# Kernel optimization log

Measured on AMD Instinct MI355X. Metric: run time of the kernel, lower is better.

The kernel has to match this reference:

```python
import jax, jax.numpy as jnp
import numpy as np

B, H, W, C = 4, 64, 64, 256
CK = C // 8          # 32, f/g projection dim
COUT = 256           # channels_out


def setup_inputs() -> dict:
    key = jax.random.key(0)
    ks = jax.random.split(key, 6)
    s = lambda fan_in: 1.0 / np.sqrt(fan_in)
    return {
        "x": jax.random.normal(ks[0], (B, H, W, C), dtype=jnp.float32),
        "Wf": jax.random.normal(ks[1], (C, CK), dtype=jnp.float32) * s(C),
        "bf": jnp.zeros((CK,), dtype=jnp.float32),
        "Wg": jax.random.normal(ks[2], (C, CK), dtype=jnp.float32) * s(C),
        "bg": jnp.zeros((CK,), dtype=jnp.float32),
        "Wh": jax.random.normal(ks[3], (C, COUT), dtype=jnp.float32) * s(C),
        "bh": jnp.zeros((COUT,), dtype=jnp.float32),
        "Wo": jax.random.normal(ks[4], (COUT, COUT), dtype=jnp.float32) * s(COUT),
        "bo": jnp.zeros((COUT,), dtype=jnp.float32),
        "gamma": jnp.zeros((1,), dtype=jnp.float32),
    }


def reference(x, Wf, bf, Wg, bg, Wh, bh, Wo, bo, gamma):
    b, h, w, c = x.shape
    n = h * w
    xf = x.reshape(b, n, c)                       # [B, N, C]
    # 1x1 convs == per-location dense projections
    f = xf @ Wf + bf                              # [B, N, CK]
    g = xf @ Wg + bg                              # [B, N, CK]
    hh = xf @ Wh + bh                             # [B, N, COUT]
    scores = jnp.einsum("bqk,bnk->bqn", f, g)    # [B, N, N]
    probs = jax.nn.softmax(scores, axis=-1)
    attn = jnp.einsum("bqn,bnd->bqd", probs, hh)  # [B, N, COUT]
    o = attn @ Wo + bo                            # [B, N, COUT]
    y = gamma * o.reshape(b, h, w, -1) + x
    return y
```

## Files before the change

### kernel.cpp

```cpp
#include <hip/hip_runtime.h>
#include <stdint.h>

typedef __attribute__((ext_vector_type(4))) float f32x4;
typedef __attribute__((ext_vector_type(2))) float f32x2;
typedef __attribute__((ext_vector_type(8))) short bf16x8;
typedef __attribute__((ext_vector_type(4))) unsigned short u16x4;

#define NB 4
#define NN 4096
#define CC 256

__device__ __forceinline__ unsigned short f2bf(float f) {
  union { float f; unsigned int u; } v; v.f = f;
  unsigned int u = v.u;
  return (unsigned short)((u + 0x7FFFu + ((u >> 16) & 1u)) >> 16);
}
__device__ __forceinline__ float bf2f(unsigned short h) {
  union { unsigned int u; float f; } v; v.u = ((unsigned int)h) << 16;
  return v.f;
}

__global__ __launch_bounds__(64) void k_wprep(
    const float* __restrict__ Wf, const float* __restrict__ Wg,
    const float* __restrict__ Wh, const float* __restrict__ Wo,
    unsigned short* __restrict__ wT, unsigned short* __restrict__ woT)
{
  const int n = blockIdx.x;
  const int l = threadIdx.x;
  const float* src; int nout, col; unsigned short* dst; int drow;
  if (n < 32)       { src = Wf; nout = 32;  col = n;       dst = wT;  drow = n; }
  else if (n < 64)  { src = Wg; nout = 32;  col = n - 32;  dst = wT;  drow = n; }
  else if (n < 320) { src = Wh; nout = 256; col = n - 64;  dst = wT;  drow = n; }
  else              { src = Wo; nout = 256; col = n - 320; dst = woT; drow = n - 320; }
  u16x4 v;
  #pragma unroll
  for (int j = 0; j < 4; ++j)
    v[j] = f2bf(src[(size_t)(4 * l + j) * nout + col]);
  *(u16x4*)&dst[(size_t)drow * 256 + 4 * l] = v;
}

__global__ __launch_bounds__(256) void k_proj(
    const float* __restrict__ x, const unsigned short* __restrict__ wT,
    const float* __restrict__ bf_, const float* __restrict__ bg_,
    const float* __restrict__ bh_,
    unsigned short* __restrict__ fo, unsigned short* __restrict__ go,
    unsigned short* __restrict__ vT)
{
  __shared__ __align__(16) unsigned short xs[32][264];

  const int t = threadIdx.x, w = t >> 6, l = t & 63;
  const int h = l >> 4, q = l & 15;
  const int bid = blockIdx.x;
  const int rt = (bid & 7) * 64 + (bid >> 3);
  const int r0 = rt * 32;

  #pragma unroll
  for (int p = 0; p < 8; ++p) {
    int idx = t + (p << 8);
    int rr = idx >> 6, c4 = (idx & 63) << 2;
    f32x4 v = *(const f32x4*)&x[(size_t)(r0 + rr) * 256 + c4];
    u16x4 o;
    #pragma unroll
    for (int j = 0; j < 4; ++j) o[j] = f2bf(v[j]);
    *(u16x4*)&xs[rr][c4] = o;
  }
  __syncthreads();

  const f32x4 zero = {0.f, 0.f, 0.f, 0.f};
  f32x4 acc[2][5];
  #pragma unroll
  for (int mf = 0; mf < 2; ++mf)
    #pragma unroll
    for (int nf = 0; nf < 5; ++nf) acc[mf][nf] = zero;

  #pragma unroll
  for (int ks = 0; ks < 8; ++ks) {
    bf16x8 a0 = *(const bf16x8*)&xs[q][ks * 32 + 8 * h];
    bf16x8 a1 = *(const bf16x8*)&xs[16 + q][ks * 32 + 8 * h];
    #pragma unroll
    for (int nf = 0; nf < 5; ++nf) {
      bf16x8 b = *(const bf16x8*)&wT[(size_t)(80 * w + 16 * nf + q) * 256 + ks * 32 + 8 * h];
      acc[0][nf] = __builtin_amdgcn_mfma_f32_16x16x32_bf16(a0, b, acc[0][nf], 0, 0, 0);
      acc[1][nf] = __builtin_amdgcn_mfma_f32_16x16x32_bf16(a1, b, acc[1][nf], 0, 0, 0);
    }
  }

  __syncthreads();

  #pragma unroll
  for (int nf = 0; nf < 5; ++nf) {
    const int colb = 80 * w + 16 * nf;
    const int colq = colb + q;
    #pragma unroll
    for (int mf = 0; mf < 2; ++mf) {
      #pragma unroll
      for (int i = 0; i < 4; ++i) {
        int lr = 16 * mf + 4 * h + i;
        float val = acc[mf][nf][i];
        if (colb < 32) {
          fo[(size_t)(r0 + lr) * 32 + colq] =
              f2bf((val + bf_[colq]) * 1.44269504088896f);
        } else if (colb < 64) {
          go[(size_t)(r0 + lr) * 32 + (colq - 32)] = f2bf(val + bg_[colq - 32]);
        } else {
          xs[lr][colq - 64] = f2bf(val + bh_[colq - 64]);
        }
      }
    }
  }
  __syncthreads();

  const int tile = rt >> 1, sfix = rt & 1;
  unsigned short* dst = vT + (size_t)tile * 16384;
  #pragma unroll
  for (int p = 0; p < 4; ++p) {
    int ci = t + (p << 8);
    int dt = ci >> 6, ll = ci & 63;
    int h2 = (ci >> 4) & 3, q2 = ci & 15;
    bf16x8 v;
    #pragma unroll
    for (int i = 0; i < 8; ++i)
      v[i] = (short)xs[8 * h2 + i][dt * 16 + q2];
    *(bf16x8*)&dst[(size_t)(dt * 128 + sfix * 64 + ll) * 8] = v;
  }
}

#define SM_FIXED_MAX 72.0f

#define ATTN_TILE(KT, VCUR, VNXT, CUR)                                          \
  {                                                                             \
                   \
    f32x4 s0 = __builtin_amdgcn_mfma_f32_16x16x32_bf16(afrag[0], bfj, zero, 0, 0, 0); \
    f32x4 s1 = __builtin_amdgcn_mfma_f32_16x16x32_bf16(afrag[1], bfj, zero, 0, 0, 0); \
    if ((KT) < 63)                                                              \
      bfj = *(const bf16x8*)&gbase[(size_t)(((KT) + 1) * 64 + jst * 16 + q) * 32 + 8 * h]; \
          \
    _Pragma("unroll")                                                           \
    for (int i = 0; i < 4; ++i) {                                               \
      float p0 = exp2f(s0[i] - SM_FIXED_MAX);                                   \
      float p1 = exp2f(s1[i] - SM_FIXED_MAX);                                   \
      lrow[0][i] += p0;                                                         \
      lrow[1][i] += p1;                                                         \
      int slot = (ph2 * 16 + 4 * h + i) * 8 + pi2;                              \
      pbuf[CUR][sec0 * 512 + slot] = (unsigned short)(__float_as_uint(p0) >> 16); \
      pbuf[CUR][sec1 * 512 + slot] = (unsigned short)(__float_as_uint(p1) >> 16); \
    }                                                                           \
    asm volatile("s_waitcnt lgkmcnt(0)" ::: "memory");                          \
    __builtin_amdgcn_s_barrier();                                               \
    __builtin_amdgcn_sched_barrier(0);                                          \
       \
    if ((KT) < 63) {                                                            \
      const unsigned short* vs = vbase + (size_t)((KT) + 1) * 16384;            \
      VNXT[0] = *(const bf16x8*)(vs + (size_t)(dt0 * 128 + l) * 8);             \
      VNXT[1] = *(const bf16x8*)(vs + (size_t)(dt0 * 128 + 64 + l) * 8);        \
      VNXT[2] = *(const bf16x8*)(vs + (size_t)(dt1 * 128 + l) * 8);             \
      VNXT[3] = *(const bf16x8*)(vs + (size_t)(dt1 * 128 + 64 + l) * 8);        \
    }                                                                           \
                             \
    __builtin_amdgcn_s_setprio(1);                                              \
    _Pragma("unroll")                                                           \
    for (int uu = 0; uu < 4; ++uu) {                                            \
      bf16x8 pa0 = *(const bf16x8*)&pbuf[CUR][(uu * 2 + 0) * 512 + l * 8];      \
      bf16x8 pa1 = *(const bf16x8*)&pbuf[CUR][(uu * 2 + 1) * 512 + l * 8];      \
      acc[uu][0] = __builtin_amdgcn_mfma_f32_16x16x32_bf16(pa0, VCUR[0], acc[uu][0], 0, 0, 0); \
      acc[uu][0] = __builtin_amdgcn_mfma_f32_16x16x32_bf16(pa1, VCUR[1], acc[uu][0], 0, 0, 0); \
      acc[uu][1] = __builtin_amdgcn_mfma_f32_16x16x32_bf16(pa0, VCUR[2], acc[uu][1], 0, 0, 0); \
      acc[uu][1] = __builtin_amdgcn_mfma_f32_16x16x32_bf16(pa1, VCUR[3], acc[uu][1], 0, 0, 0); \
    }                                                                           \
    __builtin_amdgcn_s_setprio(0);                                              \
  }

__global__ __launch_bounds__(512, 2) void k_attn(
    const unsigned short* __restrict__ fq,
    const unsigned short* __restrict__ gk,
    const unsigned short* __restrict__ vT,
    float* __restrict__ attn)
{
  __shared__ __align__(16) unsigned short pbuf[2][4096];
  __shared__ float lred[4][4][16];

  const int bid = blockIdx.x;
  const int b  = (bid & 7) >> 1;
  const int qt = (bid >> 3) + ((bid & 1) << 5);
  const int t = threadIdx.x, w = t >> 6, l = t & 63;
  const int h = l >> 4, q = l & 15;
  const int qrow = qt * 64;

  const int uh  = w & 1;
  const int jst = w >> 1;
  const int dt0 = 2 * w, dt1 = 2 * w + 1;

  bf16x8 afrag[2];
  #pragma unroll
  for (int uu = 0; uu < 2; ++uu)
    afrag[uu] = *(const bf16x8*)
        &fq[((size_t)b * NN + qrow + (2 * uh + uu) * 16 + q) * 32 + 8 * h];

  const f32x4 zero = {0.f, 0.f, 0.f, 0.f};
  f32x4 acc[4][2];
  #pragma unroll
  for (int uu = 0; uu < 4; ++uu)
    #pragma unroll
    for (int dl = 0; dl < 2; ++dl) acc[uu][dl] = zero;
  float lrow[2][4];
  #pragma unroll
  for (int uu = 0; uu < 2; ++uu)
    #pragma unroll
    for (int i = 0; i < 4; ++i) lrow[uu][i] = 0.f;

  const unsigned short* gbase = gk + (size_t)b * NN * 32;
  const unsigned short* vbase = vT + (size_t)b * 64 * 16384;

  const int kcol = jst * 16 + q;
  const int ps = kcol >> 5, ph2 = (kcol & 31) >> 3, pi2 = kcol & 7;
  const int sec0 = (2 * uh + 0) * 2 + ps;
  const int sec1 = (2 * uh + 1) * 2 + ps;

  bf16x8 vA[4], vB[4];
  vA[0] = *(const bf16x8*)(vbase + (size_t)(dt0 * 128 + l) * 8);
  vA[1] = *(const bf16x8*)(vbase + (size_t)(dt0 * 128 + 64 + l) * 8);
  vA[2] = *(const bf16x8*)(vbase + (size_t)(dt1 * 128 + l) * 8);
  vA[3] = *(const bf16x8*)(vbase + (size_t)(dt1 * 128 + 64 + l) * 8);
  bf16x8 bfj = *(const bf16x8*)&gbase[(size_t)(jst * 16 + q) * 32 + 8 * h];

  #pragma unroll 1
  for (int kt = 0; kt < 64; kt += 2) {
    ATTN_TILE(kt,     vA, vB, 0);
    ATTN_TILE(kt + 1, vB, vA, 1);
  }

  #pragma unroll
  for (int uu = 0; uu < 2; ++uu)
    #pragma unroll
    for (int i = 0; i < 4; ++i)
      #pragma unroll
      for (int d = 1; d < 16; d <<= 1)
        lrow[uu][i] += __shfl_xor(lrow[uu][i], d);

  if (q == 0) {
    #pragma unroll
    for (int uu = 0; uu < 2; ++uu)
      #pragma unroll
      for (int i = 0; i < 4; ++i)
        lred[jst][2 * uh + uu][4 * h + i] = lrow[uu][i];
  }
  __syncthreads();

  float rl[4][4];
  #pragma unroll
  for (int uu = 0; uu < 4; ++uu)
    #pragma unroll
    for (int i = 0; i < 4; ++i) {
      int row = 4 * h + i;
      rl[uu][i] = 1.0f / (lred[0][uu][row] + lred[1][uu][row] +
                          lred[2][uu][row] + lred[3][uu][row]);
    }

  #pragma unroll
  for (int uu = 0; uu < 4; ++uu)
    #pragma unroll
    for (int dl = 0; dl < 2; ++dl) {
      int dt = 2 * w + dl;
      #pragma unroll
      for (int i = 0; i < 4; ++i)
        attn[((size_t)b * NN + qrow + uu * 16 + 4 * h + i) * 256 + dt * 16 + q] =
            acc[uu][dl][i] * rl[uu][i];
    }
}

__global__ __launch_bounds__(256) void k_out(
    const unsigned short* __restrict__ woT, const float* __restrict__ bo,
    const float* __restrict__ gamma, const float* __restrict__ x,
    float* __restrict__ y)
{
  __shared__ __align__(16) unsigned short as_[32][264];

  const int t = threadIdx.x, w = t >> 6, l = t & 63;
  const int h = l >> 4, q = l & 15;
  const int bid = blockIdx.x;
  const int rt = (bid & 7) * 64 + (bid >> 3);
  const int r0 = rt * 32;

  #pragma unroll
  for (int p = 0; p < 8; ++p) {
    int idx = t + (p << 8);
    int rr = idx >> 6, c4 = (idx & 63) << 2;
    f32x4 v = *(const f32x4*)&y[(size_t)(r0 + rr) * 256 + c4];
    u16x4 o;
    #pragma unroll
    for (int j = 0; j < 4; ++j) o[j] = f2bf(v[j]);
    *(u16x4*)&as_[rr][c4] = o;
  }
  __syncthreads();

  const f32x4 zero = {0.f, 0.f, 0.f, 0.f};
  f32x4 acc[2][4];
  #pragma unroll
  for (int mf = 0; mf < 2; ++mf)
    #pragma unroll
    for (int nf = 0; nf < 4; ++nf) acc[mf][nf] = zero;

  #pragma unroll
  for (int ks = 0; ks < 8; ++ks) {
    bf16x8 a0 = *(const bf16x8*)&as_[q][ks * 32 + 8 * h];
    bf16x8 a1 = *(const bf16x8*)&as_[16 + q][ks * 32 + 8 * h];
    #pragma unroll
    for (int nf = 0; nf < 4; ++nf) {
      bf16x8 b = *(const bf16x8*)&woT[(size_t)(64 * w + 16 * nf + q) * 256 + ks * 32 + 8 * h];
      acc[0][nf] = __builtin_amdgcn_mfma_f32_16x16x32_bf16(a0, b, acc[0][nf], 0, 0, 0);
      acc[1][nf] = __builtin_amdgcn_mfma_f32_16x16x32_bf16(a1, b, acc[1][nf], 0, 0, 0);
    }
  }

  const float gm = gamma[0];
  #pragma unroll
  for (int mf = 0; mf < 2; ++mf)
    #pragma unroll
    for (int nf = 0; nf < 4; ++nf) {
      int col = 64 * w + 16 * nf + q;
      #pragma unroll
      for (int i = 0; i < 4; ++i) {
        size_t off = (size_t)(r0 + 16 * mf + 4 * h + i) * 256 + col;
        y[off] = gm * (acc[mf][nf][i] + bo[col]) + x[off];
      }
    }
}

extern "C" void kernel_launch(void* const* d_in, const int* in_sizes, int n_in,
                              void* d_out, int out_size, void* d_ws, size_t ws_size,
                              hipStream_t stream) {
  const float* x     = (const float*)d_in[0];
  const float* Wf    = (const float*)d_in[1];
  const float* bf_   = (const float*)d_in[2];
  const float* Wg    = (const float*)d_in[3];
  const float* bg_   = (const float*)d_in[4];
  const float* Wh    = (const float*)d_in[5];
  const float* bh_   = (const float*)d_in[6];
  const float* Wo    = (const float*)d_in[7];
  const float* bo    = (const float*)d_in[8];
  const float* gamma = (const float*)d_in[9];

  unsigned short* f   = (unsigned short*)d_ws;
  unsigned short* g   = f   + (size_t)16384 * 32;
  unsigned short* vT  = g   + (size_t)16384 * 32;
  unsigned short* wT  = vT  + (size_t)16384 * 256;
  unsigned short* woT = wT  + (size_t)320 * 256;

  float* attn = (float*)d_out;

  k_wprep<<<576, 64, 0, stream>>>(Wf, Wg, Wh, Wo, wT, woT);
  k_proj<<<512, 256, 0, stream>>>(x, wT, bf_, bg_, bh_, f, g, vT);
  k_attn<<<256, 512, 0, stream>>>(f, g, vT, attn);
  k_out<<<512, 256, 0, stream>>>(woT, bo, gamma, x, attn);
}
```

Measured before the change: 109.1 us.

## Process two key tiles per barrier, stagger tile order, pass bf16 attn to out-proj

The attention loop now handles two 64-key tiles per step, which halves the number of LDS barriers. It prefetches both V tiles and both G fragments for the next step before the softmax work, and starts each block's key sweep at an offset based on its query tile so blocks touch different K/V tiles at the same time. The attention output is written as bf16 to a workspace buffer instead of fp32 into the output tensor, so k_out loads half as many bytes and skips its conversion. In exchange it doubles the LDS P buffer and raises register pressure from eight V fragments per buffer, which may lower occupancy.

```diff
diff --git a/kernel.cpp b/kernel.cpp
--- a/kernel.cpp
+++ b/kernel.cpp
@@ -127,45 +127,64 @@
 
 #define SM_FIXED_MAX 72.0f
 
-#define ATTN_TILE(KT, VCUR, VNXT, CUR)                                          \
+#define ATTN_STEP(ST, VP, VN, GP, GN, CUR)                                      \
   {                                                                             \
-                   \
-    f32x4 s0 = __builtin_amdgcn_mfma_f32_16x16x32_bf16(afrag[0], bfj, zero, 0, 0, 0); \
-    f32x4 s1 = __builtin_amdgcn_mfma_f32_16x16x32_bf16(afrag[1], bfj, zero, 0, 0, 0); \
-    if ((KT) < 63)                                                              \
-      bfj = *(const bf16x8*)&gbase[(size_t)(((KT) + 1) * 64 + jst * 16 + q) * 32 + 8 * h]; \
-          \
+                                                    \
+    f32x4 sA0 = __builtin_amdgcn_mfma_f32_16x16x32_bf16(afrag[0], GP[0], zero, 0, 0, 0); \
+    f32x4 sA1 = __builtin_amdgcn_mfma_f32_16x16x32_bf16(afrag[1], GP[0], zero, 0, 0, 0); \
+    f32x4 sB0 = __builtin_amdgcn_mfma_f32_16x16x32_bf16(afrag[0], GP[1], zero, 0, 0, 0); \
+    f32x4 sB1 = __builtin_amdgcn_mfma_f32_16x16x32_bf16(afrag[1], GP[1], zero, 0, 0, 0); \
+                                   \
+    if ((ST) + 1 < 32) {                                                        \
+      const int kA = (2 * (ST) + 2 + qt) & 63;                                  \
+      const int kB = (2 * (ST) + 3 + qt) & 63;                                  \
+      const unsigned short* vsA = vbase + (size_t)kA * 16384;                   \
+      const unsigned short* vsB = vbase + (size_t)kB * 16384;                   \
+      VN[0] = *(const bf16x8*)(vsA + (size_t)(dt0 * 128 + l) * 8);              \
+      VN[1] = *(const bf16x8*)(vsA + (size_t)(dt0 * 128 + 64 + l) * 8);         \
+      VN[2] = *(const bf16x8*)(vsA + (size_t)(dt1 * 128 + l) * 8);              \
+      VN[3] = *(const bf16x8*)(vsA + (size_t)(dt1 * 128 + 64 + l) * 8);         \
+      VN[4] = *(const bf16x8*)(vsB + (size_t)(dt0 * 128 + l) * 8);              \
+      VN[5] = *(const bf16x8*)(vsB + (size_t)(dt0 * 128 + 64 + l) * 8);         \
+      VN[6] = *(const bf16x8*)(vsB + (size_t)(dt1 * 128 + l) * 8);              \
+      VN[7] = *(const bf16x8*)(vsB + (size_t)(dt1 * 128 + 64 + l) * 8);         \
+      GN[0] = *(const bf16x8*)&gbase[(size_t)(kA * 64 + jst * 16 + q) * 32 + 8 * h]; \
+      GN[1] = *(const bf16x8*)&gbase[(size_t)(kB * 64 + jst * 16 + q) * 32 + 8 * h]; \
+    }                                                                           \
+                     \
     _Pragma("unroll")                                                           \
     for (int i = 0; i < 4; ++i) {                                               \
-      float p0 = exp2f(s0[i] - SM_FIXED_MAX);                                   \
-      float p1 = exp2f(s1[i] - SM_FIXED_MAX);                                   \
-      lrow[0][i] += p0;                                                         \
-      lrow[1][i] += p1;                                                         \
+      float pA0 = exp2f(sA0[i] - SM_FIXED_MAX);                                 \
+      float pA1 = exp2f(sA1[i] - SM_FIXED_MAX);                                 \
+      float pB0 = exp2f(sB0[i] - SM_FIXED_MAX);                                 \
+      float pB1 = exp2f(sB1[i] - SM_FIXED_MAX);                                 \
+      lrow[0][i] += pA0 + pB0;                                                  \
+      lrow[1][i] += pA1 + pB1;                                                  \
       int slot = (ph2 * 16 + 4 * h + i) * 8 + pi2;                              \
-      pbuf[CUR][sec0 * 512 + slot] = (unsigned short)(__float_as_uint(p0) >> 16); \
-      pbuf[CUR][sec1 * 512 + slot] = (unsigned short)(__float_as_uint(p1) >> 16); \
+      pbuf[CUR][sec0 * 512 + slot]        = (unsigned short)(__float_as_uint(pA0) >> 16); \
+      pbuf[CUR][sec1 * 512 + slot]        = (unsigned short)(__float_as_uint(pA1) >> 16); \
+      pbuf[CUR][4096 + sec0 * 512 + slot] = (unsigned short)(__float_as_uint(pB0) >> 16); \
+      pbuf[CUR][4096 + sec1 * 512 + slot] = (unsigned short)(__float_as_uint(pB1) >> 16); \
     }                                                                           \
     asm volatile("s_waitcnt lgkmcnt(0)" ::: "memory");                          \
     __builtin_amdgcn_s_barrier();                                               \
     __builtin_amdgcn_sched_barrier(0);                                          \
-       \
-    if ((KT) < 63) {                                                            \
-      const unsigned short* vs = vbase + (size_t)((KT) + 1) * 16384;            \
-      VNXT[0] = *(const bf16x8*)(vs + (size_t)(dt0 * 128 + l) * 8);             \
-      VNXT[1] = *(const bf16x8*)(vs + (size_t)(dt0 * 128 + 64 + l) * 8);        \
-      VNXT[2] = *(const bf16x8*)(vs + (size_t)(dt1 * 128 + l) * 8);             \
-      VNXT[3] = *(const bf16x8*)(vs + (size_t)(dt1 * 128 + 64 + l) * 8);        \
-    }                                                                           \
-                             \
+             \
     __builtin_amdgcn_s_setprio(1);                                              \
     _Pragma("unroll")                                                           \
     for (int uu = 0; uu < 4; ++uu) {                                            \
-      bf16x8 pa0 = *(const bf16x8*)&pbuf[CUR][(uu * 2 + 0) * 512 + l * 8];      \
-      bf16x8 pa1 = *(const bf16x8*)&pbuf[CUR][(uu * 2 + 1) * 512 + l * 8];      \
-      acc[uu][0] = __builtin_amdgcn_mfma_f32_16x16x32_bf16(pa0, VCUR[0], acc[uu][0], 0, 0, 0); \
-      acc[uu][0] = __builtin_amdgcn_mfma_f32_16x16x32_bf16(pa1, VCUR[1], acc[uu][0], 0, 0, 0); \
-      acc[uu][1] = __builtin_amdgcn_mfma_f32_16x16x32_bf16(pa0, VCUR[2], acc[uu][1], 0, 0, 0); \
-      acc[uu][1] = __builtin_amdgcn_mfma_f32_16x16x32_bf16(pa1, VCUR[3], acc[uu][1], 0, 0, 0); \
+      bf16x8 paA0 = *(const bf16x8*)&pbuf[CUR][(uu * 2 + 0) * 512 + l * 8];     \
+      bf16x8 paA1 = *(const bf16x8*)&pbuf[CUR][(uu * 2 + 1) * 512 + l * 8];     \
+      bf16x8 paB0 = *(const bf16x8*)&pbuf[CUR][4096 + (uu * 2 + 0) * 512 + l * 8]; \
+      bf16x8 paB1 = *(const bf16x8*)&pbuf[CUR][4096 + (uu * 2 + 1) * 512 + l * 8]; \
+      acc[uu][0] = __builtin_amdgcn_mfma_f32_16x16x32_bf16(paA0, VP[0], acc[uu][0], 0, 0, 0); \
+      acc[uu][0] = __builtin_amdgcn_mfma_f32_16x16x32_bf16(paA1, VP[1], acc[uu][0], 0, 0, 0); \
+      acc[uu][0] = __builtin_amdgcn_mfma_f32_16x16x32_bf16(paB0, VP[4], acc[uu][0], 0, 0, 0); \
+      acc[uu][0] = __builtin_amdgcn_mfma_f32_16x16x32_bf16(paB1, VP[5], acc[uu][0], 0, 0, 0); \
+      acc[uu][1] = __builtin_amdgcn_mfma_f32_16x16x32_bf16(paA0, VP[2], acc[uu][1], 0, 0, 0); \
+      acc[uu][1] = __builtin_amdgcn_mfma_f32_16x16x32_bf16(paA1, VP[3], acc[uu][1], 0, 0, 0); \
+      acc[uu][1] = __builtin_amdgcn_mfma_f32_16x16x32_bf16(paB0, VP[6], acc[uu][1], 0, 0, 0); \
+      acc[uu][1] = __builtin_amdgcn_mfma_f32_16x16x32_bf16(paB1, VP[7], acc[uu][1], 0, 0, 0); \
     }                                                                           \
     __builtin_amdgcn_s_setprio(0);                                              \
   }
@@ -174,9 +193,9 @@
     const unsigned short* __restrict__ fq,
     const unsigned short* __restrict__ gk,
     const unsigned short* __restrict__ vT,
-    float* __restrict__ attn)
+    unsigned short* __restrict__ ab)
 {
-  __shared__ __align__(16) unsigned short pbuf[2][4096];
+  __shared__ __align__(16) unsigned short pbuf[2][8192];
   __shared__ float lred[4][4][16];
 
   const int bid = blockIdx.x;
@@ -216,17 +235,27 @@
   const int sec0 = (2 * uh + 0) * 2 + ps;
   const int sec1 = (2 * uh + 1) * 2 + ps;
 
-  bf16x8 vA[4], vB[4];
-  vA[0] = *(const bf16x8*)(vbase + (size_t)(dt0 * 128 + l) * 8);
-  vA[1] = *(const bf16x8*)(vbase + (size_t)(dt0 * 128 + 64 + l) * 8);
-  vA[2] = *(const bf16x8*)(vbase + (size_t)(dt1 * 128 + l) * 8);
-  vA[3] = *(const bf16x8*)(vbase + (size_t)(dt1 * 128 + 64 + l) * 8);
-  bf16x8 bfj = *(const bf16x8*)&gbase[(size_t)(jst * 16 + q) * 32 + 8 * h];
+  const int kp0 = qt & 63, kp1 = (qt + 1) & 63;
+  bf16x8 vX[8], vY[8], gX[2], gY[2];
+  {
+    const unsigned short* vsA = vbase + (size_t)kp0 * 16384;
+    const unsigned short* vsB = vbase + (size_t)kp1 * 16384;
+    vX[0] = *(const bf16x8*)(vsA + (size_t)(dt0 * 128 + l) * 8);
+    vX[1] = *(const bf16x8*)(vsA + (size_t)(dt0 * 128 + 64 + l) * 8);
+    vX[2] = *(const bf16x8*)(vsA + (size_t)(dt1 * 128 + l) * 8);
+    vX[3] = *(const bf16x8*)(vsA + (size_t)(dt1 * 128 + 64 + l) * 8);
+    vX[4] = *(const bf16x8*)(vsB + (size_t)(dt0 * 128 + l) * 8);
+    vX[5] = *(const bf16x8*)(vsB + (size_t)(dt0 * 128 + 64 + l) * 8);
+    vX[6] = *(const bf16x8*)(vsB + (size_t)(dt1 * 128 + l) * 8);
+    vX[7] = *(const bf16x8*)(vsB + (size_t)(dt1 * 128 + 64 + l) * 8);
+    gX[0] = *(const bf16x8*)&gbase[(size_t)(kp0 * 64 + jst * 16 + q) * 32 + 8 * h];
+    gX[1] = *(const bf16x8*)&gbase[(size_t)(kp1 * 64 + jst * 16 + q) * 32 + 8 * h];
+  }
 
   #pragma unroll 1
-  for (int kt = 0; kt < 64; kt += 2) {
-    ATTN_TILE(kt,     vA, vB, 0);
-    ATTN_TILE(kt + 1, vB, vA, 1);
+  for (int st = 0; st < 32; st += 2) {
+    ATTN_STEP(st,     vX, vY, gX, gY, 0);
+    ATTN_STEP(st + 1, vY, vX, gY, gX, 1);
   }
 
   #pragma unroll
@@ -263,15 +292,15 @@
       int dt = 2 * w + dl;
       #pragma unroll
       for (int i = 0; i < 4; ++i)
-        attn[((size_t)b * NN + qrow + uu * 16 + 4 * h + i) * 256 + dt * 16 + q] =
-            acc[uu][dl][i] * rl[uu][i];
+        ab[((size_t)b * NN + qrow + uu * 16 + 4 * h + i) * 256 + dt * 16 + q] =
+            f2bf(acc[uu][dl][i] * rl[uu][i]);
     }
 }
 
 __global__ __launch_bounds__(256) void k_out(
     const unsigned short* __restrict__ woT, const float* __restrict__ bo,
     const float* __restrict__ gamma, const float* __restrict__ x,
-    float* __restrict__ y)
+    const unsigned short* __restrict__ ab, float* __restrict__ y)
 {
   __shared__ __align__(16) unsigned short as_[32][264];
 
@@ -282,14 +311,10 @@
   const int r0 = rt * 32;
 
   #pragma unroll
-  for (int p = 0; p < 8; ++p) {
+  for (int p = 0; p < 4; ++p) {
     int idx = t + (p << 8);
-    int rr = idx >> 6, c4 = (idx & 63) << 2;
-    f32x4 v = *(const f32x4*)&y[(size_t)(r0 + rr) * 256 + c4];
-    u16x4 o;
-    #pragma unroll
-    for (int j = 0; j < 4; ++j) o[j] = f2bf(v[j]);
-    *(u16x4*)&as_[rr][c4] = o;
+    int rr = idx >> 5, c8 = (idx & 31) << 3;
+    *(bf16x8*)&as_[rr][c8] = *(const bf16x8*)&ab[(size_t)(r0 + rr) * 256 + c8];
   }
   __syncthreads();
 
@@ -343,13 +368,14 @@
   unsigned short* f   = (unsigned short*)d_ws;
   unsigned short* g   = f   + (size_t)16384 * 32;
   unsigned short* vT  = g   + (size_t)16384 * 32;
-  unsigned short* wT  = vT  + (size_t)16384 * 256;
+  unsigned short* ab  = vT  + (size_t)16384 * 256;
+  unsigned short* wT  = ab  + (size_t)16384 * 256;
   unsigned short* woT = wT  + (size_t)320 * 256;
 
-  float* attn = (float*)d_out;
+  float* y = (float*)d_out;
 
   k_wprep<<<576, 64, 0, stream>>>(Wf, Wg, Wh, Wo, wT, woT);
   k_proj<<<512, 256, 0, stream>>>(x, wT, bf_, bg_, bh_, f, g, vT);
-  k_attn<<<256, 512, 0, stream>>>(f, g, vT, attn);
-  k_out<<<512, 256, 0, stream>>>(woT, bo, gamma, x, attn);
-}
+  k_attn<<<256, 512, 0, stream>>>(f, g, vT, ab);
+  k_out<<<512, 256, 0, stream>>>(woT, bo, gamma, x, ab, y);
+}
```

After: 99.08 us. -9.2%, faster.
